# Performance work log

Hardware: AMD Instinct MI355X
Metric: run time of the kernel (lower is better)

The kernel has to match this reference:

```python
import jax, jax.numpy as jnp
import numpy as np
from jax import lax

CONF_THRES = 0.25
IOU_THRES = 0.45
MAX_DET = 300      # detections kept after NMS
TOPK = 1024        # candidates entering NMS (sorted by score)
MAX_WH = 7680.0    # class offset for class-aware NMS
NC = 80            # classes
NM = 32            # mask prototypes
IMG = 640          # network input size
PROTO_HW = 160     # proto map resolution (IMG/4)
EPS = 1e-7


def xywh2xyxy(x):
    cx, cy, w, h = x[:, 0], x[:, 1], x[:, 2], x[:, 3]
    return jnp.stack([cx - w / 2, cy - h / 2, cx + w / 2, cy + h / 2], axis=1)


def box_iou(box1, box2):
    # box1: [K,4], box2: [M,4] in xyxy -> [K,M]
    a1, a2 = box1[:, None, :2], box1[:, None, 2:]
    b1, b2 = box2[None, :, :2], box2[None, :, 2:]
    inter = jnp.clip(jnp.minimum(a2, b2) - jnp.maximum(a1, b1), 0).prod(-1)
    area1 = (a2 - a1).prod(-1)
    area2 = (b2 - b1).prod(-1)
    return inter / (area1 + area2 - inter + EPS)


def greedy_nms_keep(boxes, valid, iou_thres):
    # boxes already sorted by descending score; returns bool keep mask [K]
    K = boxes.shape[0]
    sup = box_iou(boxes, boxes) > iou_thres  # [K,K]
    lower = jnp.arange(K)

    def body(i, keep):
        suppressed = jnp.any(keep & sup[:, i] & (lower < i))
        return keep.at[i].set(valid[i] & ~suppressed)

    return lax.fori_loop(0, K, body, jnp.zeros((K,), dtype=bool))


def setup_inputs() -> dict:
    key = jax.random.key(0)
    k1, k2, k3, k4, k5, k6 = jax.random.split(key, 6)
    N = 25200
    cxcy = jax.random.uniform(k1, (1, N, 2), jnp.float32, 0.0, float(IMG))
    wh = jax.random.uniform(k2, (1, N, 2), jnp.float32, 5.0, 120.0)
    obj = jax.random.uniform(k3, (1, N, 1), jnp.float32)
    cls = jax.random.uniform(k4, (1, N, NC), jnp.float32)
    coef = jax.random.normal(k5, (1, N, NM), jnp.float32) * 0.5
    prediction = jnp.concatenate([cxcy, wh, obj, cls, coef], axis=2)  # [1,N,117]
    protos = jax.random.normal(k6, (NM, PROTO_HW, PROTO_HW), jnp.float32)
    return {"prediction": prediction, "protos": protos}


def reference(prediction, protos):
    x = prediction[0]                       # [N, 5+NC+NM]
    obj = x[:, 4]
    cls_conf = x[:, 5:5 + NC] * obj[:, None]  # x[:,5:] *= x[:,4:5]
    conf = cls_conf.max(axis=1)
    j = jnp.argmax(cls_conf, axis=1)
    valid_all = (obj > CONF_THRES) & (conf > CONF_THRES)

    boxes_all = xywh2xyxy(x[:, :4])
    scores_masked = jnp.where(valid_all, conf, -1.0)
    top_scores, idx = lax.top_k(scores_masked, TOPK)  # sorted descending

    b = boxes_all[idx]              # [TOPK,4], no class offset
    cls_id = j[idx]                 # [TOPK]
    coef = x[idx, 5 + NC:]          # [TOPK,NM]
    valid = top_scores > CONF_THRES

    nms_boxes = b + (cls_id.astype(b.dtype) * MAX_WH)[:, None]  # class-aware
    keep = greedy_nms_keep(nms_boxes, valid, IOU_THRES)

    keep_scores = jnp.where(keep, top_scores, -1.0)
    fs, i2 = lax.top_k(keep_scores, MAX_DET)
    fvalid = fs > CONF_THRES
    fb = b[i2] * fvalid[:, None].astype(b.dtype)
    fcls = jnp.where(fvalid, cls_id[i2], -1)
    fcoef = coef[i2] * fvalid[:, None].astype(coef.dtype)
    fs = jnp.where(fvalid, fs, 0.0)

    # process_mask_native
    m = jax.nn.sigmoid(fcoef @ protos.reshape(NM, -1))          # [MAX_DET, HW*HW]
    m = m.reshape(MAX_DET, PROTO_HW, PROTO_HW)
    m = jax.image.resize(m, (MAX_DET, IMG, IMG), method='bilinear')
    x1, y1, x2, y2 = fb[:, 0], fb[:, 1], fb[:, 2], fb[:, 3]
    r = jnp.arange(IMG, dtype=fb.dtype)[None, None, :]  # along width vs x
    c = jnp.arange(IMG, dtype=fb.dtype)[None, :, None]  # along height vs y
    crop = ((r >= x1[:, None, None]) & (r < x2[:, None, None]) &
            (c >= y1[:, None, None]) & (c < y2[:, None, None]))
    masks_f = m * crop.astype(m.dtype) * fvalid[:, None, None].astype(m.dtype)
    masks_bool = masks_f > 0.5
    return masks_f, masks_bool, fb, fs, fcls
```

## Files before the change

### kernel.cpp

```cpp
#include <hip/hip_runtime.h>

constexpr int   kNA     = 25200;
constexpr int   kStride = 117;
constexpr int   kNC     = 80;
constexpr int   kNM     = 32;
constexpr int   kTopK   = 1024;
constexpr int   kMaxDet = 300;
constexpr int   kImg    = 640;
constexpr int   kPHW    = 160;
constexpr float kConfT  = 0.25f;
constexpr float kIouT   = 0.45f;
constexpr float kMaxWH  = 7680.0f;

constexpr unsigned long long kMaskElems = 300ull * 640ull * 640ull;

typedef float v4f __attribute__((ext_vector_type(4)));

constexpr size_t O_SCORES = 0;
constexpr size_t O_BOXES  = 100864;
constexpr size_t O_CLS    = 504064;
constexpr size_t O_TKIDX  = 604864;
constexpr size_t O_TKSC   = 608960;
constexpr size_t O_TKBOX  = 613056;
constexpr size_t O_TKNBOX = 629440;
constexpr size_t O_TKCLS  = 645824;
constexpr size_t O_SUP    = 649984;
constexpr size_t O_NDET   = 782336;
constexpr size_t O_DBOX   = 782400;
constexpr size_t O_DCOEF  = 787264;

constexpr int kDecRows = 128;
__global__ __launch_bounds__(128) void decode_k(const float* __restrict__ pred,
        float* __restrict__ scores, float* __restrict__ boxes, int* __restrict__ cls) {
    __shared__ float rows[kDecRows * kStride];
    int base = blockIdx.x * kDecRows;
    int nrows = min(kDecRows, kNA - base);
    int total = nrows * kStride;
    const float* src = pred + (size_t)base * kStride;
    for (int i = threadIdx.x; i < total; i += kDecRows) rows[i] = src[i];
    __syncthreads();
    int r = threadIdx.x;
    if (r >= nrows) return;
    int a = base + r;
    const float* p = rows + r * kStride;
    float obj = p[4];
    float best = -1.0f; int bj = 0;
    for (int c = 0; c < kNC; ++c) {
        float v = p[5 + c] * obj;
        if (v > best) { best = v; bj = c; }
    }
    bool valid = (obj > kConfT) && (best > kConfT);
    scores[a] = valid ? best : -1.0f;
    float cx = p[0], cy = p[1], w = p[2], h = p[3];
    float hw = w * 0.5f, hh = h * 0.5f;
    boxes[4*a+0] = cx - hw; boxes[4*a+1] = cy - hh;
    boxes[4*a+2] = cx + hw; boxes[4*a+3] = cy + hh;
    cls[a] = bj;
}

__device__ __forceinline__ unsigned f2ord(float f) {
    unsigned b = __float_as_uint(f);
    return (b & 0x80000000u) ? ~b : (b | 0x80000000u);
}
__device__ __forceinline__ float ord2f(unsigned u) {
    unsigned b = (u & 0x80000000u) ? (u ^ 0x80000000u) : ~u;
    return __uint_as_float(b);
}

__global__ __launch_bounds__(1024) void topk_k(const float* __restrict__ scores,
        const float* __restrict__ boxes, const int* __restrict__ cls,
        int* __restrict__ tk_idx, float* __restrict__ tk_sc, float* __restrict__ tk_box,
        float* __restrict__ tk_nbox, int* __restrict__ tk_cls) {
    __shared__ unsigned long long keys[kTopK];
    __shared__ int wcnt[16];
    __shared__ int sh_tot;
    __shared__ unsigned sh_cnt;
    int tid = threadIdx.x;
    int lane = tid & 63, wid = tid >> 6;

    unsigned uv[25];
#pragma unroll
    for (int k = 0; k < 25; ++k) {
        int i = tid + k * 1024;
        uv[k] = (i < kNA) ? f2ord(scores[i]) : 0u;
    }

    unsigned lo = 0, hi = 0xFFFFFFFFu;
    for (int it = 0; it < 32; ++it) {
        unsigned mid = (unsigned)(((unsigned long long)lo + (unsigned long long)hi) >> 1);
        if (mid == lo) break;
        int c = 0;
#pragma unroll
        for (int k = 0; k < 25; ++k) c += (uv[k] >= mid);
#pragma unroll
        for (int off = 32; off >= 1; off >>= 1) c += __shfl_down(c, off);
        if (lane == 0) wcnt[wid] = c;
        __syncthreads();
        if (tid == 0) { int t = 0; for (int w = 0; w < 16; ++w) t += wcnt[w]; sh_tot = t; }
        __syncthreads();
        int tot = sh_tot;
        if (tot >= kTopK) lo = mid; else hi = mid;
    }
    unsigned uT = lo;

    {
        int c = 0;
#pragma unroll
        for (int k = 0; k < 25; ++k) c += (uv[k] >= uT + 1u);
#pragma unroll
        for (int off = 32; off >= 1; off >>= 1) c += __shfl_down(c, off);
        if (lane == 0) wcnt[wid] = c;
        __syncthreads();
        if (tid == 0) { int t = 0; for (int w = 0; w < 16; ++w) t += wcnt[w]; sh_tot = t; }
        __syncthreads();
    }
    int krem = kTopK - sh_tot;
    if (tid == 0) sh_cnt = 0;
    __syncthreads();

#pragma unroll
    for (int k = 0; k < 25; ++k) {
        int i = tid + k * 1024;
        unsigned u = uv[k];
        if (i < kNA && u > uT) {
            unsigned p = atomicAdd(&sh_cnt, 1u);
            keys[p] = ((unsigned long long)u << 32) | (unsigned)(~i);
        }
    }
    __syncthreads();

    int ilo = 0, ihi = kNA;
    while (ilo < ihi) {
        int mid = (ilo + ihi) >> 1;
        int c = 0;
#pragma unroll
        for (int k = 0; k < 25; ++k) {
            int i = tid + k * 1024;
            c += (i < mid && uv[k] == uT);
        }
#pragma unroll
        for (int off = 32; off >= 1; off >>= 1) c += __shfl_down(c, off);
        if (lane == 0) wcnt[wid] = c;
        __syncthreads();
        if (tid == 0) { int t = 0; for (int w = 0; w < 16; ++w) t += wcnt[w]; sh_tot = t; }
        __syncthreads();
        int cc = sh_tot;
        __syncthreads();
        if (cc >= krem) ihi = mid; else ilo = mid + 1;
    }
#pragma unroll
    for (int k = 0; k < 25; ++k) {
        int i = tid + k * 1024;
        if (i < ilo && uv[k] == uT) {
            unsigned p = atomicAdd(&sh_cnt, 1u);
            keys[p] = ((unsigned long long)uT << 32) | (unsigned)(~i);
        }
    }
    __syncthreads();

    for (int k2 = 2; k2 <= kTopK; k2 <<= 1) {
        for (int j = k2 >> 1; j > 0; j >>= 1) {
            int partner = tid ^ j;
            unsigned long long a = keys[tid], b = keys[partner];
            bool iLower = (tid & j) == 0;
            bool descRegion = (tid & k2) == 0;
            unsigned long long mx = (a > b) ? a : b;
            unsigned long long mn = (a > b) ? b : a;
            unsigned long long res = (iLower == descRegion) ? mx : mn;
            __syncthreads();
            keys[tid] = res;
            __syncthreads();
        }
    }

    unsigned long long key = keys[tid];
    unsigned u = (unsigned)(key >> 32);
    int idx = (int)(~((unsigned)key));
    tk_idx[tid] = idx;
    tk_sc[tid]  = ord2f(u);
    float4 bx = ((const float4*)boxes)[idx];
    ((float4*)tk_box)[tid] = bx;
    int cid = cls[idx];
    float off = (float)cid * kMaxWH;
    float4 nb; nb.x = bx.x + off; nb.y = bx.y + off; nb.z = bx.z + off; nb.w = bx.w + off;
    ((float4*)tk_nbox)[tid] = nb;
    tk_cls[tid] = cid;
}

__global__ __launch_bounds__(256) void supmat_k(const float* __restrict__ tk_nbox,
                                                unsigned long long* __restrict__ sup) {
    __shared__ float4 bxs[kTopK];
    int tid = threadIdx.x;
    for (int k = tid; k < kTopK; k += 256) bxs[k] = ((const float4*)tk_nbox)[k];
    __syncthreads();
    int r = tid >> 4, w = tid & 15;
    int i = blockIdx.x * 16 + r;
    float4 a = bxs[i];
    float areaA = (a.z - a.x) * (a.w - a.y);
    unsigned long long bits = 0;
    for (int l = 0; l < 64; ++l) {
        float4 b = bxs[w * 64 + l];
        float xx1 = fmaxf(a.x, b.x), yy1 = fmaxf(a.y, b.y);
        float xx2 = fminf(a.z, b.z), yy2 = fminf(a.w, b.w);
        float iw = fmaxf(xx2 - xx1, 0.f), ih = fmaxf(yy2 - yy1, 0.f);
        float inter = iw * ih;
        float areaB = (b.z - b.x) * (b.w - b.y);
        float iou = inter / (areaA + areaB - inter + 1e-7f);
        if (iou > kIouT) bits |= 1ull << l;
    }
    sup[(size_t)i * 16 + w] = bits;
}

__global__ __launch_bounds__(256) void nms_k(const float* __restrict__ pred,
        const float* __restrict__ tk_sc, const int* __restrict__ tk_idx,
        const float* __restrict__ tk_box, const int* __restrict__ tk_cls,
        const unsigned long long* __restrict__ sup,
        int* __restrict__ ndet, float* __restrict__ out,
        float* __restrict__ dbox, float* __restrict__ dcoef) {
    __shared__ unsigned long long buf[2][1024];
    __shared__ int dslot_lds[kMaxDet];
    __shared__ int sh_nd;
    int tid = threadIdx.x;
    int lane = tid & 63;

    unsigned long long vW = 0;
    if (tid < 64) {
        for (int b = 0; b < 16; ++b) {
            unsigned long long bw = __ballot(tk_sc[b * 64 + lane] > kConfT);
            if (lane == b) vW = bw;
        }
    }
    for (int i = tid; i < 1024; i += 256) buf[0][i] = sup[i];

    unsigned long long supW = 0;
    unsigned long long kws[16];
    for (int b = 0; b < 16; ++b) {
        __syncthreads();
        if (tid >= 64) {
            if (b + 1 < 16) {
                for (int i = tid - 64; i < 1024; i += 192)
                    buf[(b + 1) & 1][i] = sup[(size_t)(b + 1) * 1024 + i];
            }
        } else {
            const unsigned long long* ch = buf[b & 1];
            unsigned long long s  = __shfl(supW, b);
            unsigned long long vb = __shfl(vW, b);
            unsigned long long kw = 0;
            unsigned long long rbuf[8];
            int w16 = lane & 15;
#pragma unroll
            for (int p = 0; p < 8; ++p) rbuf[p] = ch[p * 16 + w16];
            for (int l = 0; l < 64; ++l) {
                unsigned long long rw = rbuf[l & 7];
                if (l + 8 < 64) rbuf[l & 7] = ch[(l + 8) * 16 + w16];
                unsigned long long rb = __shfl(rw, b);
                bool kp = ((vb >> l) & 1ull) && !((s >> l) & 1ull);
                if (kp) { kw |= 1ull << l; s |= rb; supW |= rw; }
            }
            kws[b] = kw;
        }
    }
    if (tid == 0) {
        int d = 0;
        for (int b = 0; b < 16 && d < kMaxDet; ++b) {
            unsigned long long kw = kws[b];
            for (int l = 0; l < 64 && d < kMaxDet; ++l)
                if ((kw >> l) & 1ull) dslot_lds[d++] = b * 64 + l;
        }
        sh_nd = d;
        *ndet = d;
    }
    __syncthreads();

    int n = sh_nd;
    float* fb   = out + 2 * kMaskElems;
    float* fs   = fb + kMaxDet * 4;
    float* fcls = fs + kMaxDet;
    for (int d = tid; d < kMaxDet; d += 256) {
        if (d < n) {
            int t = dslot_lds[d];
            int a = tk_idx[t];
            float4 bx = ((const float4*)tk_box)[t];
            fb[4*d+0] = bx.x; fb[4*d+1] = bx.y; fb[4*d+2] = bx.z; fb[4*d+3] = bx.w;
            fs[d] = tk_sc[t];
            fcls[d] = (float)tk_cls[t];
            ((float4*)dbox)[d] = bx;
            const float* cp = pred + (size_t)a * kStride + 5 + kNC;
            for (int c = 0; c < kNM; ++c) dcoef[d * kNM + c] = cp[c];
        } else {
            fb[4*d+0] = 0.f; fb[4*d+1] = 0.f; fb[4*d+2] = 0.f; fb[4*d+3] = 0.f;
            fs[d] = 0.f; fcls[d] = -1.0f;
            float4 z; z.x = z.y = z.z = z.w = 0.f;
            ((float4*)dbox)[d] = z;
            for (int c = 0; c < kNM; ++c) dcoef[d * kNM + c] = 0.f;
        }
    }
}

constexpr int kSliceRows = 80;
constexpr int kNSlice    = 8;
constexpr int kPatchH    = 24;
constexpr int kPatchW    = 40;

__global__ __launch_bounds__(256) void mask_k(const float* __restrict__ protos,
        const float* __restrict__ dbox, const float* __restrict__ dcoef,
        const int* __restrict__ ndet, float* __restrict__ out) {
    int d = blockIdx.x;
    int s = blockIdx.y;
    int tid = threadIdx.x;
    int r0 = s * kSliceRows;
    float* mf = out + (size_t)d * (kImg * kImg) + (size_t)r0 * kImg;
    float* mb = out + kMaskElems + (size_t)d * (kImg * kImg) + (size_t)r0 * kImg;

    bool valid = d < *ndet;
    float4 bx;
    if (valid) bx = ((const float4*)dbox)[d]; else { bx.x = bx.y = bx.z = bx.w = 0.f; }
    float x1 = bx.x, y1 = bx.y, x2 = bx.z, y2 = bx.w;

    int iy_lo = max(r0, (int)floorf(y1));
    int iy_hi = min(r0 + kSliceRows - 1, min(kImg - 1, (int)ceilf(y2)));
    int jx_lo = max(0, (int)floorf(x1));
    int jx_hi = min(kImg - 1, (int)ceilf(x2));
    bool any = valid && (iy_lo <= iy_hi) && (jx_lo <= jx_hi);

    __shared__ float coef[kNM];
    __shared__ float patch[kPatchH * kPatchW];
    int py_lo = 0, px_lo = 0, pw = 1;
    if (any) {
        py_lo = min(159, max(0, (int)floorf(((float)iy_lo + 0.5f) * 0.25f - 0.5f)));
        int py_hi = min(159, max(0, (int)floorf(((float)iy_hi + 0.5f) * 0.25f - 0.5f) + 1));
        px_lo = min(159, max(0, (int)floorf(((float)jx_lo + 0.5f) * 0.25f - 0.5f)));
        int px_hi = min(159, max(0, (int)floorf(((float)jx_hi + 0.5f) * 0.25f - 0.5f) + 1));
        int ph = py_hi - py_lo + 1; pw = px_hi - px_lo + 1;
        if (ph > kPatchH) ph = kPatchH;
        if (pw > kPatchW) pw = kPatchW;
        if (tid < kNM) coef[tid] = dcoef[d * kNM + tid];
        __syncthreads();
        int cells = ph * pw;
        for (int c = tid; c < cells; c += 256) {
            int py = py_lo + c / pw, px = px_lo + c % pw;
            const float* pp = protos + (size_t)py * kPHW + px;
            float z = 0.f;
#pragma unroll
            for (int m = 0; m < kNM; ++m) z = fmaf(coef[m], pp[(size_t)m * kPHW * kPHW], z);
            patch[c] = 1.0f / (1.0f + expf(-z));
        }
        __syncthreads();
    }

    constexpr int QPR = kImg / 4;
    for (int q = tid; q < kSliceRows * QPR; q += 256) {
        int row = q / QPR;
        int i = r0 + row;
        int j0 = (q - row * QPR) * 4;
        v4f vf = 0.f;
        v4f vb = 0.f;
        float fi = (float)i;
        if (any && fi >= y1 && fi < y2) {
            float sy = fminf(fmaxf(((float)i + 0.5f) * 0.25f - 0.5f, 0.f), 159.f);
            int yy0 = (int)sy; float fy = sy - (float)yy0;
            int yy1i = min(yy0 + 1, 159);
            const float* prow0 = &patch[(yy0 - py_lo) * pw - px_lo];
            const float* prow1 = &patch[(yy1i - py_lo) * pw - px_lo];
#pragma unroll
            for (int t = 0; t < 4; ++t) {
                int j = j0 + t; float fj = (float)j;
                if (fj >= x1 && fj < x2) {
                    float sx = fminf(fmaxf(((float)j + 0.5f) * 0.25f - 0.5f, 0.f), 159.f);
                    int xx0 = (int)sx; float fx = sx - (float)xx0;
                    int xx1i = min(xx0 + 1, 159);
                    float v00 = prow0[xx0], v01 = prow0[xx1i];
                    float v10 = prow1[xx0], v11 = prow1[xx1i];
                    float top = (1.f - fx) * v00 + fx * v01;
                    float bot = (1.f - fx) * v10 + fx * v11;
                    float m = (1.f - fy) * top + fy * bot;
                    vf[t] = m;
                    vb[t] = (m > 0.5f) ? 1.f : 0.f;
                }
            }
        }
        __builtin_nontemporal_store(vf, (v4f*)(mf + q * 4));
        __builtin_nontemporal_store(vb, (v4f*)(mb + q * 4));
    }
}

extern "C" void kernel_launch(void* const* d_in, const int* in_sizes, int n_in,
                              void* d_out, int out_size, void* d_ws, size_t ws_size,
                              hipStream_t stream) {
    const float* pred   = (const float*)d_in[0];
    const float* protos = (const float*)d_in[1];
    float* out = (float*)d_out;
    char* ws = (char*)d_ws;

    float* s_scores = (float*)(ws + O_SCORES);
    float* s_boxes  = (float*)(ws + O_BOXES);
    int*   s_cls    = (int*)  (ws + O_CLS);
    int*   tk_idx   = (int*)  (ws + O_TKIDX);
    float* tk_sc    = (float*)(ws + O_TKSC);
    float* tk_box   = (float*)(ws + O_TKBOX);
    float* tk_nbox  = (float*)(ws + O_TKNBOX);
    int*   tk_cls   = (int*)  (ws + O_TKCLS);
    unsigned long long* sup = (unsigned long long*)(ws + O_SUP);
    int*   ndet     = (int*)  (ws + O_NDET);
    float* dbox     = (float*)(ws + O_DBOX);
    float* dcoef    = (float*)(ws + O_DCOEF);

    decode_k<<<dim3((kNA + kDecRows - 1) / kDecRows), dim3(kDecRows), 0, stream>>>(pred, s_scores, s_boxes, s_cls);
    topk_k<<<dim3(1), dim3(1024), 0, stream>>>(s_scores, s_boxes, s_cls,
                                               tk_idx, tk_sc, tk_box, tk_nbox, tk_cls);
    supmat_k<<<dim3(64), dim3(256), 0, stream>>>(tk_nbox, sup);
    nms_k<<<dim3(1), dim3(256), 0, stream>>>(pred, tk_sc, tk_idx, tk_box, tk_cls, sup,
                                             ndet, out, dbox, dcoef);
    mask_k<<<dim3(300, kNSlice), dim3(256), 0, stream>>>(protos, dbox, dcoef, ndet, out);
}
```

Before: 1.228 ms.

## Zero mask outputs in bulk and write only box regions per detection

Adds a grid-stride kernel that zero-fills both mask outputs with nontemporal vector stores. The sliced mask kernel is replaced by one block per detection, which computes the proto patch once and writes interpolated values only inside the box. This removes the per-slice proto recomputation and the crop checks on every pixel, but adds a separate full-output zero pass and scattered scalar stores inside boxes. It also changes the decode block shape and makes every thread in topk read the per-wave counts itself instead of waiting on a thread-0 reduction.

```diff
diff --git a/kernel.cpp b/kernel.cpp
--- a/kernel.cpp
+++ b/kernel.cpp
@@ -29,15 +29,24 @@
 constexpr size_t O_DBOX   = 782400;
 constexpr size_t O_DCOEF  = 787264;
 
-constexpr int kDecRows = 128;
-__global__ __launch_bounds__(128) void decode_k(const float* __restrict__ pred,
+__global__ __launch_bounds__(256) void zero_k(float* __restrict__ out) {
+    const size_t n4 = (2ull * kMaskElems) >> 2;
+    const size_t stride = (size_t)gridDim.x * 256;
+    v4f z = 0.f;
+    for (size_t i = (size_t)blockIdx.x * 256 + threadIdx.x; i < n4; i += stride)
+        __builtin_nontemporal_store(z, ((v4f*)out) + i);
+}
+
+constexpr int kDecRows = 64;
+constexpr int kDecThr  = 128;
+__global__ __launch_bounds__(kDecThr) void decode_k(const float* __restrict__ pred,
         float* __restrict__ scores, float* __restrict__ boxes, int* __restrict__ cls) {
     __shared__ float rows[kDecRows * kStride];
     int base = blockIdx.x * kDecRows;
     int nrows = min(kDecRows, kNA - base);
     int total = nrows * kStride;
     const float* src = pred + (size_t)base * kStride;
-    for (int i = threadIdx.x; i < total; i += kDecRows) rows[i] = src[i];
+    for (int i = threadIdx.x; i < total; i += kDecThr) rows[i] = src[i];
     __syncthreads();
     int r = threadIdx.x;
     if (r >= nrows) return;
@@ -73,7 +82,6 @@
         float* __restrict__ tk_nbox, int* __restrict__ tk_cls) {
     __shared__ unsigned long long keys[kTopK];
     __shared__ int wcnt[16];
-    __shared__ int sh_tot;
     __shared__ unsigned sh_cnt;
     int tid = threadIdx.x;
     int lane = tid & 63, wid = tid >> 6;
@@ -94,27 +102,32 @@
         for (int k = 0; k < 25; ++k) c += (uv[k] >= mid);
 #pragma unroll
         for (int off = 32; off >= 1; off >>= 1) c += __shfl_down(c, off);
+        __syncthreads();
         if (lane == 0) wcnt[wid] = c;
         __syncthreads();
-        if (tid == 0) { int t = 0; for (int w = 0; w < 16; ++w) t += wcnt[w]; sh_tot = t; }
-        __syncthreads();
-        int tot = sh_tot;
+        int tot = 0;
+#pragma unroll
+        for (int w = 0; w < 16; ++w) tot += wcnt[w];
         if (tot >= kTopK) lo = mid; else hi = mid;
     }
     unsigned uT = lo;
 
+    int nGreater;
     {
         int c = 0;
 #pragma unroll
         for (int k = 0; k < 25; ++k) c += (uv[k] >= uT + 1u);
 #pragma unroll
         for (int off = 32; off >= 1; off >>= 1) c += __shfl_down(c, off);
+        __syncthreads();
         if (lane == 0) wcnt[wid] = c;
         __syncthreads();
-        if (tid == 0) { int t = 0; for (int w = 0; w < 16; ++w) t += wcnt[w]; sh_tot = t; }
-        __syncthreads();
-    }
-    int krem = kTopK - sh_tot;
+        int t = 0;
+#pragma unroll
+        for (int w = 0; w < 16; ++w) t += wcnt[w];
+        nGreater = t;
+    }
+    int krem = kTopK - nGreater;
     if (tid == 0) sh_cnt = 0;
     __syncthreads();
 
@@ -127,7 +140,6 @@
             keys[p] = ((unsigned long long)u << 32) | (unsigned)(~i);
         }
     }
-    __syncthreads();
 
     int ilo = 0, ihi = kNA;
     while (ilo < ihi) {
@@ -140,12 +152,12 @@
         }
 #pragma unroll
         for (int off = 32; off >= 1; off >>= 1) c += __shfl_down(c, off);
+        __syncthreads();
         if (lane == 0) wcnt[wid] = c;
         __syncthreads();
-        if (tid == 0) { int t = 0; for (int w = 0; w < 16; ++w) t += wcnt[w]; sh_tot = t; }
-        __syncthreads();
-        int cc = sh_tot;
-        __syncthreads();
+        int cc = 0;
+#pragma unroll
+        for (int w = 0; w < 16; ++w) cc += wcnt[w];
         if (cc >= krem) ihi = mid; else ilo = mid + 1;
     }
 #pragma unroll
@@ -297,90 +309,71 @@
     }
 }
 
-constexpr int kSliceRows = 80;
-constexpr int kNSlice    = 8;
-constexpr int kPatchH    = 24;
-constexpr int kPatchW    = 40;
-
-__global__ __launch_bounds__(256) void mask_k(const float* __restrict__ protos,
+constexpr int kPatch = 34;
+
+__global__ __launch_bounds__(256) void patch_k(const float* __restrict__ protos,
         const float* __restrict__ dbox, const float* __restrict__ dcoef,
         const int* __restrict__ ndet, float* __restrict__ out) {
     int d = blockIdx.x;
-    int s = blockIdx.y;
+    if (d >= *ndet) return;
+    float4 bx = ((const float4*)dbox)[d];
+    float x1 = bx.x, y1 = bx.y, x2 = bx.z, y2 = bx.w;
+
+    int i_lo = max(0, (int)ceilf(y1));
+    int i_hi = min(kImg - 1, (int)ceilf(y2) - 1);
+    int j_lo = max(0, (int)ceilf(x1));
+    int j_hi = min(kImg - 1, (int)ceilf(x2) - 1);
+    if (i_lo > i_hi || j_lo > j_hi) return;
+
+    int py_lo = min(159, max(0, (int)floorf(((float)i_lo + 0.5f) * 0.25f - 0.5f)));
+    int py_hi = min(159, max(0, (int)floorf(((float)i_hi + 0.5f) * 0.25f - 0.5f) + 1));
+    int px_lo = min(159, max(0, (int)floorf(((float)j_lo + 0.5f) * 0.25f - 0.5f)));
+    int px_hi = min(159, max(0, (int)floorf(((float)j_hi + 0.5f) * 0.25f - 0.5f) + 1));
+    int ph = py_hi - py_lo + 1, pw = px_hi - px_lo + 1;
+    if (ph > kPatch) ph = kPatch;
+    if (pw > kPatch) pw = kPatch;
+
     int tid = threadIdx.x;
-    int r0 = s * kSliceRows;
-    float* mf = out + (size_t)d * (kImg * kImg) + (size_t)r0 * kImg;
-    float* mb = out + kMaskElems + (size_t)d * (kImg * kImg) + (size_t)r0 * kImg;
-
-    bool valid = d < *ndet;
-    float4 bx;
-    if (valid) bx = ((const float4*)dbox)[d]; else { bx.x = bx.y = bx.z = bx.w = 0.f; }
-    float x1 = bx.x, y1 = bx.y, x2 = bx.z, y2 = bx.w;
-
-    int iy_lo = max(r0, (int)floorf(y1));
-    int iy_hi = min(r0 + kSliceRows - 1, min(kImg - 1, (int)ceilf(y2)));
-    int jx_lo = max(0, (int)floorf(x1));
-    int jx_hi = min(kImg - 1, (int)ceilf(x2));
-    bool any = valid && (iy_lo <= iy_hi) && (jx_lo <= jx_hi);
-
     __shared__ float coef[kNM];
-    __shared__ float patch[kPatchH * kPatchW];
-    int py_lo = 0, px_lo = 0, pw = 1;
-    if (any) {
-        py_lo = min(159, max(0, (int)floorf(((float)iy_lo + 0.5f) * 0.25f - 0.5f)));
-        int py_hi = min(159, max(0, (int)floorf(((float)iy_hi + 0.5f) * 0.25f - 0.5f) + 1));
-        px_lo = min(159, max(0, (int)floorf(((float)jx_lo + 0.5f) * 0.25f - 0.5f)));
-        int px_hi = min(159, max(0, (int)floorf(((float)jx_hi + 0.5f) * 0.25f - 0.5f) + 1));
-        int ph = py_hi - py_lo + 1; pw = px_hi - px_lo + 1;
-        if (ph > kPatchH) ph = kPatchH;
-        if (pw > kPatchW) pw = kPatchW;
-        if (tid < kNM) coef[tid] = dcoef[d * kNM + tid];
-        __syncthreads();
-        int cells = ph * pw;
-        for (int c = tid; c < cells; c += 256) {
-            int py = py_lo + c / pw, px = px_lo + c % pw;
-            const float* pp = protos + (size_t)py * kPHW + px;
-            float z = 0.f;
-#pragma unroll
-            for (int m = 0; m < kNM; ++m) z = fmaf(coef[m], pp[(size_t)m * kPHW * kPHW], z);
-            patch[c] = 1.0f / (1.0f + expf(-z));
-        }
-        __syncthreads();
-    }
-
-    constexpr int QPR = kImg / 4;
-    for (int q = tid; q < kSliceRows * QPR; q += 256) {
-        int row = q / QPR;
-        int i = r0 + row;
-        int j0 = (q - row * QPR) * 4;
-        v4f vf = 0.f;
-        v4f vb = 0.f;
-        float fi = (float)i;
-        if (any && fi >= y1 && fi < y2) {
-            float sy = fminf(fmaxf(((float)i + 0.5f) * 0.25f - 0.5f, 0.f), 159.f);
-            int yy0 = (int)sy; float fy = sy - (float)yy0;
-            int yy1i = min(yy0 + 1, 159);
-            const float* prow0 = &patch[(yy0 - py_lo) * pw - px_lo];
-            const float* prow1 = &patch[(yy1i - py_lo) * pw - px_lo];
-#pragma unroll
-            for (int t = 0; t < 4; ++t) {
-                int j = j0 + t; float fj = (float)j;
-                if (fj >= x1 && fj < x2) {
-                    float sx = fminf(fmaxf(((float)j + 0.5f) * 0.25f - 0.5f, 0.f), 159.f);
-                    int xx0 = (int)sx; float fx = sx - (float)xx0;
-                    int xx1i = min(xx0 + 1, 159);
-                    float v00 = prow0[xx0], v01 = prow0[xx1i];
-                    float v10 = prow1[xx0], v11 = prow1[xx1i];
-                    float top = (1.f - fx) * v00 + fx * v01;
-                    float bot = (1.f - fx) * v10 + fx * v11;
-                    float m = (1.f - fy) * top + fy * bot;
-                    vf[t] = m;
-                    vb[t] = (m > 0.5f) ? 1.f : 0.f;
-                }
-            }
-        }
-        __builtin_nontemporal_store(vf, (v4f*)(mf + q * 4));
-        __builtin_nontemporal_store(vb, (v4f*)(mb + q * 4));
+    __shared__ float patch[kPatch * kPatch];
+    if (tid < kNM) coef[tid] = dcoef[d * kNM + tid];
+    __syncthreads();
+    int cells = ph * pw;
+    for (int c = tid; c < cells; c += 256) {
+        int py = py_lo + c / pw, px = px_lo + c % pw;
+        const float* pp = protos + (size_t)py * kPHW + px;
+        float z = 0.f;
+#pragma unroll
+        for (int m = 0; m < kNM; ++m) z = fmaf(coef[m], pp[(size_t)m * kPHW * kPHW], z);
+        patch[c] = 1.0f / (1.0f + expf(-z));
+    }
+    __syncthreads();
+
+    float* mf = out + (size_t)d * (kImg * kImg);
+    float* mb = out + kMaskElems + (size_t)d * (kImg * kImg);
+    int W = j_hi - j_lo + 1;
+    int H = i_hi - i_lo + 1;
+    int dr = tid >> 7, dc = tid & 127;
+    for (int rr = dr; rr < H; rr += 2) {
+        int i = i_lo + rr;
+        float sy = fminf(fmaxf(((float)i + 0.5f) * 0.25f - 0.5f, 0.f), 159.f);
+        int yy0 = (int)sy; float fy = sy - (float)yy0;
+        int yy1i = min(yy0 + 1, 159);
+        const float* prow0 = &patch[(yy0 - py_lo) * pw - px_lo];
+        const float* prow1 = &patch[(yy1i - py_lo) * pw - px_lo];
+        for (int cc = dc; cc < W; cc += 128) {
+            int j = j_lo + cc;
+            float sx = fminf(fmaxf(((float)j + 0.5f) * 0.25f - 0.5f, 0.f), 159.f);
+            int xx0 = (int)sx; float fx = sx - (float)xx0;
+            int xx1i = min(xx0 + 1, 159);
+            float v00 = prow0[xx0], v01 = prow0[xx1i];
+            float v10 = prow1[xx0], v11 = prow1[xx1i];
+            float top = (1.f - fx) * v00 + fx * v01;
+            float bot = (1.f - fx) * v10 + fx * v11;
+            float m = (1.f - fy) * top + fy * bot;
+            mf[(size_t)i * kImg + j] = m;
+            mb[(size_t)i * kImg + j] = (m > 0.5f) ? 1.f : 0.f;
+        }
     }
 }
 
@@ -405,11 +398,12 @@
     float* dbox     = (float*)(ws + O_DBOX);
     float* dcoef    = (float*)(ws + O_DCOEF);
 
-    decode_k<<<dim3((kNA + kDecRows - 1) / kDecRows), dim3(kDecRows), 0, stream>>>(pred, s_scores, s_boxes, s_cls);
+    zero_k<<<dim3(2048), dim3(256), 0, stream>>>(out);
+    decode_k<<<dim3((kNA + kDecRows - 1) / kDecRows), dim3(kDecThr), 0, stream>>>(pred, s_scores, s_boxes, s_cls);
     topk_k<<<dim3(1), dim3(1024), 0, stream>>>(s_scores, s_boxes, s_cls,
                                                tk_idx, tk_sc, tk_box, tk_nbox, tk_cls);
     supmat_k<<<dim3(64), dim3(256), 0, stream>>>(tk_nbox, sup);
     nms_k<<<dim3(1), dim3(256), 0, stream>>>(pred, tk_sc, tk_idx, tk_box, tk_cls, sup,
                                              ndet, out, dbox, dcoef);
-    mask_k<<<dim3(300, kNSlice), dim3(256), 0, stream>>>(protos, dbox, dcoef, ndet, out);
-}
+    patch_k<<<dim3(kMaxDet), dim3(256), 0, stream>>>(protos, dbox, dcoef, ndet, out);
+}
```

New measurement: 1.289 ms. 1.05x slower.
